# Kernel optimization log

Measured on AMD Instinct MI355X. Metric: run time of the kernel, lower is better.

## Reference

```python
import jax, jax.numpy as jnp
import numpy as np

B = 64           # number of graphs
MAXN = 128       # max nodes per graph (== to_dense_batch n)
D = 512          # hidden_dim
H = 16           # n_attn_heads
HS = D // H      # head_size
SCALE = HS ** -0.5
EPS = 1e-5

# deterministic ragged node counts in [64,128], max exactly 128
_COUNTS = 64 + (np.arange(B) * 37) % 65
NTOT = int(_COUNTS.sum())  # 6148


def setup_inputs() -> dict:
    key = jax.random.key(0)
    ks = jax.random.split(key, 10)
    r = D ** -0.5  # uniform init radius used by the module

    def lin(k):
        kw, kb = jax.random.split(k)
        W = jax.random.uniform(kw, (D, D), minval=-r, maxval=r, dtype=jnp.float32)
        b = jax.random.uniform(kb, (D,), minval=-r, maxval=r, dtype=jnp.float32)
        return W, b

    Wq, bq = lin(ks[0])
    Wk, bk = lin(ks[1])
    Wv, bv = lin(ks[2])
    Wp, bp = lin(ks[3])
    x = jax.random.normal(ks[4], (NTOT, D), dtype=jnp.float32)
    attn_bias = 0.1 * jax.random.normal(ks[5], (B, H, MAXN, MAXN), dtype=jnp.float32)
    batch = jnp.asarray(np.repeat(np.arange(B), _COUNTS), dtype=jnp.int32)
    return {
        "x": x, "attn_bias": attn_bias,
        "Wq": Wq, "bq": bq, "Wk": Wk, "bk": bk, "Wv": Wv, "bv": bv,
        "Wp": Wp, "bp": bp,
        "ln_w": jnp.ones((D,), jnp.float32), "ln_b": jnp.zeros((D,), jnp.float32),
        "batch": batch,
    }


def reference(x, attn_bias, Wq, bq, Wk, bk, Wv, bv, Wp, bp, ln_w, ln_b, batch):
    # eval-mode BiasedSelfAttentionLayer (all dropouts are identity)
    Bn, Hh, n, _ = attn_bias.shape
    N = x.shape[0]
    # to_dense_batch: per-node position inside its graph
    counts = jax.ops.segment_sum(jnp.ones(N, jnp.int32), batch, num_segments=Bn)
    starts = jnp.cumsum(counts) - counts
    pos = jnp.arange(N) - starts[batch]
    x_dense = jnp.zeros((Bn, n, D), x.dtype).at[batch, pos].set(x)  # [B,n,D]
    mask = jnp.zeros((Bn, n), bool).at[batch, pos].set(True)        # [B,n]

    def heads(W, b):
        return (x_dense @ W.T + b).reshape(Bn, n, Hh, HS).transpose(0, 2, 1, 3)

    q = heads(Wq, bq)  # [B,H,n,hs]
    k = heads(Wk, bk)
    v = heads(Wv, bv)

    attn = jnp.einsum("bhqd,bhkd->bhqk", q, k) * SCALE + attn_bias  # [B,H,n,n]
    mask2 = mask[:, None, :, None]  # valid queries
    mask3 = mask[:, None, None, :]  # valid keys
    attn = jnp.where(mask3, attn, -jnp.inf)   # masked_fill(~mask3, -inf)
    attn = jnp.where(mask2, attn, 0.0)        # masked_fill(~mask2, 0.0)
    attn = jax.nn.softmax(attn, axis=-1)
    attn = jnp.where(mask2, attn, 0.0)        # re-zero invalid query rows

    out = jnp.einsum("bhqk,bhkd->bhqd", attn, v)           # [B,H,n,hs]
    out = out.transpose(0, 2, 1, 3).reshape(Bn, n, D)      # [B,n,D]
    out = out @ Wp.T + bp
    out = out[batch, pos] + x                               # scatter back + residual
    # LayerNorm
    mu = out.mean(-1, keepdims=True)
    var = out.var(-1, keepdims=True)
    return (out - mu) / jnp.sqrt(var + EPS) * ln_w + ln_b
```

## Files before the change

kernel.cpp:

```cpp
#include <hip/hip_runtime.h>
#include <math.h>

#define NTOT 6148
#define NB 64
#define DM 512
#define SCALE_F 0.17677669529663687f

typedef __attribute__((ext_vector_type(8))) short bf16x8;
typedef __attribute__((ext_vector_type(4))) float f32x4;

__device__ __forceinline__ short f2bf(float f) {
  union { float f; unsigned u; } v; v.f = f;
  unsigned r = (v.u + 0x7fffu + ((v.u >> 16) & 1u)) >> 16;
  return (short)r;
}

__device__ __forceinline__ void gl_lds16(const void* g, void* l) {
  auto gp = (const __attribute__((address_space(1))) unsigned*)(unsigned long long)(uintptr_t)g;
  auto lp = (__attribute__((address_space(3))) unsigned*)(unsigned long long)(uintptr_t)l;
  __builtin_amdgcn_global_load_lds(gp, lp, 16, 0, 0);
}

__global__ __launch_bounds__(256) void k_starts(const int* __restrict__ batch,
                                                int* __restrict__ starts) {
  int i = blockIdx.x * 256 + threadIdx.x;
  if (i >= NTOT) return;
  int b = batch[i];
  if (i == 0) starts[b] = 0;
  else if (batch[i - 1] != b) starts[b] = i;
  if (i == NTOT - 1) starts[NB] = NTOT;
}

__global__ __launch_bounds__(256) void k_cvt(const float* __restrict__ x,
                                             const float* __restrict__ wq,
                                             const float* __restrict__ wk,
                                             const float* __restrict__ wv,
                                             const float* __restrict__ wp,
                                             short* __restrict__ xb,
                                             short* __restrict__ wqb,
                                             short* __restrict__ wkb,
                                             short* __restrict__ wvb,
                                             short* __restrict__ wpb) {
  const int bid = blockIdx.x;
  const float* s; short* d; long off;
  if (bid < 1537) {
    s = x; d = xb;
    off = ((long)bid * 256 + threadIdx.x) * 8;
  } else {
    int wi = (bid - 1537) >> 7;
    s = (wi == 0) ? wq : (wi == 1) ? wk : (wi == 2) ? wv : wp;
    d = (wi == 0) ? wqb : (wi == 1) ? wkb : (wi == 2) ? wvb : wpb;
    off = ((long)((bid - 1537) & 127) * 256 + threadIdx.x) * 8;
  }
  float4 v0 = *(const float4*)(s + off);
  float4 v1 = *(const float4*)(s + off + 4);
  bf16x8 o;
  o[0] = f2bf(v0.x); o[1] = f2bf(v0.y); o[2] = f2bf(v0.z); o[3] = f2bf(v0.w);
  o[4] = f2bf(v1.x); o[5] = f2bf(v1.y); o[6] = f2bf(v1.z); o[7] = f2bf(v1.w);
  *(bf16x8*)(d + off) = o;
}

template <int NT, bool BF16OUT>
__global__ __launch_bounds__(256) void k_gemm_mfma(
    const short* __restrict__ Abf,
    const short* __restrict__ W0, const short* __restrict__ W1, const short* __restrict__ W2,
    const float* __restrict__ b0, const float* __restrict__ b1, const float* __restrict__ b2,
    const float* __restrict__ resid, void* __restrict__ Cv, int ldc, int M) {
  constexpr int NF = NT / 32;
  __shared__ __align__(16) short As[2][64][32];
  __shared__ __align__(16) short Bs[2][NT][32];
  const int tid = threadIdx.x;
  const int w = tid >> 6, l = tid & 63;
  const int m0 = blockIdx.y * 64;
  const int n0 = blockIdx.x * NT;
  const int sel = n0 >> 9;
  const short* Wt = (sel == 0) ? W0 : (sel == 1) ? W1 : W2;
  const float* bt = (sel == 0) ? b0 : (sel == 1) ? b1 : b2;
  const int nl0 = n0 & 511;
  const int wr = w >> 1, wc = w & 1;
  const int lr = l >> 2;
  const int lc = (l & 3) * 8;
  const int fr = l & 15, fs = (l >> 4) * 8;

  const long gaA = (long)min(m0 + w * 16 + lr, M - 1) * 512 + lc;
  const long gaB0 = (long)(nl0 + ((NT == 128) ? w * 32 : w * 16) + lr) * 512 + lc;
  const long gaB1 = (long)(nl0 + w * 32 + 16 + lr) * 512 + lc;

  f32x4 acc[2][NF];
#pragma unroll
  for (int m = 0; m < 2; m++)
#pragma unroll
    for (int n = 0; n < NF; n++) acc[m][n] = (f32x4){0.f, 0.f, 0.f, 0.f};

  auto stage = [&](int kt, int buf) {
    const int k0 = kt * 32;
    gl_lds16(Abf + gaA + k0, &As[buf][w * 16][0]);
    if (NT == 128) {
      gl_lds16(Wt + gaB0 + k0, &Bs[buf][w * 32][0]);
      gl_lds16(Wt + gaB1 + k0, &Bs[buf][w * 32 + 16][0]);
    } else {
      gl_lds16(Wt + gaB0 + k0, &Bs[buf][w * 16][0]);
    }
  };
  auto compute = [&](int buf) {
    bf16x8 af[2], bfr[NF];
#pragma unroll
    for (int m = 0; m < 2; m++) af[m] = *(const bf16x8*)&As[buf][wr * 32 + m * 16 + fr][fs];
#pragma unroll
    for (int n = 0; n < NF; n++)
      bfr[n] = *(const bf16x8*)&Bs[buf][wc * (NT / 2) + n * 16 + fr][fs];
#pragma unroll
    for (int m = 0; m < 2; m++)
#pragma unroll
      for (int n = 0; n < NF; n++)
        acc[m][n] = __builtin_amdgcn_mfma_f32_16x16x32_bf16(af[m], bfr[n], acc[m][n], 0, 0, 0);
  };

  stage(0, 0);
  __syncthreads();
  for (int step = 0; step < 16; step++) {
    if (step < 15) stage(step + 1, (step + 1) & 1);
    compute(step & 1);
    __syncthreads();
  }

  const int er = (l >> 4) * 4, ec = l & 15;
#pragma unroll
  for (int n = 0; n < NF; n++) {
    const int col = n0 + wc * (NT / 2) + n * 16 + ec;
    const float bv = bt[col & 511];
#pragma unroll
    for (int m = 0; m < 2; m++) {
      const int rowb = m0 + wr * 32 + m * 16 + er;
#pragma unroll
      for (int j = 0; j < 4; j++) {
        const int row = rowb + j;
        if (row < M) {
          float v = acc[m][n][j] + bv;
          if (resid) v += resid[(long)row * 512 + col];
          if (BF16OUT) ((short*)Cv)[(long)row * ldc + col] = f2bf(v);
          else ((float*)Cv)[(long)row * ldc + col] = v;
        }
      }
    }
  }
}

__global__ __launch_bounds__(256, 2) void k_attn(const short* __restrict__ QKVbf,
                                                 const float* __restrict__ bias,
                                                 const int* __restrict__ starts,
                                                 short* __restrict__ Obf) {
  __shared__ __align__(16) float BiasP[4][16][264];
  __shared__ __align__(16) short Vtb[32][136];
  const int h = blockIdx.x, b = blockIdx.y;
  const int s0 = starts[b], cnt = starts[b + 1] - s0;
  const int tid = threadIdx.x, l = tid & 63, w = tid >> 6;
  const int wq0 = w * 32;
  const int lg = l >> 4, lk = l & 15, fs = lg * 8;
  const bool active = wq0 < cnt;
  short* Pw = (short*)&BiasP[w][0][0];

  const int u = l >> 2, c = (l & 3) * 8;
  const short* vbase = QKVbf + 1024 + h * 32 + c;
  const bf16x8 v0 = *(const bf16x8*)(vbase + (long)(s0 + min(wq0 + u, cnt - 1)) * 1536);
  const bf16x8 v1 = *(const bf16x8*)(vbase + (long)(s0 + min(wq0 + u + 16, cnt - 1)) * 1536);

  const float* bbase = bias + ((long)(b * 16 + h) << 14);
  if (active) {
    const float* bsrc = bbase + (long)wq0 * 128 + l * 4;
#pragma unroll
    for (int t = 0; t < 16; t++)
      gl_lds16(bsrc + t * 256, &BiasP[w][t][0]);
  }

  bf16x8 aq[2], bk[8];
  if (active) {
    const short* qbase = QKVbf + h * 32 + fs;
#pragma unroll
    for (int m = 0; m < 2; m++)
      aq[m] = *(const bf16x8*)(qbase + (long)(s0 + min(wq0 + m * 16 + lk, cnt - 1)) * 1536);
#pragma unroll
    for (int n = 0; n < 8; n++)
      bk[n] = *(const bf16x8*)(qbase + 512 + (long)(s0 + min(n * 16 + lk, cnt - 1)) * 1536);
  }

#pragma unroll
  for (int i = 0; i < 8; i++) Vtb[c + i][wq0 + u] = v0[i];
#pragma unroll
  for (int i = 0; i < 8; i++) Vtb[c + i][wq0 + u + 16] = v1[i];

  f32x4 S[2][8];
  float invs[2][4];
  if (active) {
#pragma unroll
    for (int n = 0; n < 8; n++)
#pragma unroll
      for (int m = 0; m < 2; m++)
        S[m][n] = __builtin_amdgcn_mfma_f32_16x16x32_bf16(aq[m], bk[n],
                                                          (f32x4){0.f, 0.f, 0.f, 0.f}, 0, 0, 0);
    asm volatile("s_waitcnt vmcnt(0)" ::: "memory");
    __builtin_amdgcn_sched_barrier(0);

#pragma unroll
    for (int m = 0; m < 2; m++) {
      const int rb = m * 16 + lg * 4;
#pragma unroll
      for (int n = 0; n < 8; n++) {
        const int k = n * 16 + lk;
        const bool kok = k < cnt;
#pragma unroll
        for (int j = 0; j < 4; j++) {
          const int r = rb + j;
          const float sv = S[m][n][j] * SCALE_F + BiasP[w][r >> 1][(r & 1) * 128 + k];
          S[m][n][j] = kok ? sv : -1e30f;
        }
      }
#pragma unroll
      for (int j = 0; j < 4; j++) {
        float mx = S[m][0][j];
#pragma unroll
        for (int n = 1; n < 8; n++) mx = fmaxf(mx, S[m][n][j]);
        mx = fmaxf(mx, __shfl_xor(mx, 1));
        mx = fmaxf(mx, __shfl_xor(mx, 2));
        mx = fmaxf(mx, __shfl_xor(mx, 4));
        mx = fmaxf(mx, __shfl_xor(mx, 8));
        float sum = 0.f;
#pragma unroll
        for (int n = 0; n < 8; n++) {
          const float p = __expf(S[m][n][j] - mx);
          S[m][n][j] = p;
          sum += p;
        }
        sum += __shfl_xor(sum, 1);
        sum += __shfl_xor(sum, 2);
        sum += __shfl_xor(sum, 4);
        sum += __shfl_xor(sum, 8);
        invs[m][j] = 1.f / sum;
        const int r = rb + j;
#pragma unroll
        for (int n = 0; n < 8; n++) Pw[r * 136 + n * 16 + lk] = f2bf(S[m][n][j]);
      }
    }
  }

  __syncthreads();
  if (!active) return;

  f32x4 O[2][2];
#pragma unroll
  for (int m = 0; m < 2; m++)
#pragma unroll
    for (int dt = 0; dt < 2; dt++) O[m][dt] = (f32x4){0.f, 0.f, 0.f, 0.f};
#pragma unroll
  for (int kc = 0; kc < 4; kc++) {
    bf16x8 pa[2], vb[2];
#pragma unroll
    for (int m = 0; m < 2; m++)
      pa[m] = *(const bf16x8*)&Pw[(m * 16 + lk) * 136 + kc * 32 + fs];
#pragma unroll
    for (int dt = 0; dt < 2; dt++) vb[dt] = *(const bf16x8*)&Vtb[dt * 16 + lk][kc * 32 + fs];
#pragma unroll
    for (int m = 0; m < 2; m++)
#pragma unroll
      for (int dt = 0; dt < 2; dt++)
        O[m][dt] = __builtin_amdgcn_mfma_f32_16x16x32_bf16(pa[m], vb[dt], O[m][dt], 0, 0, 0);
  }
#pragma unroll
  for (int m = 0; m < 2; m++) {
    const int qb0 = wq0 + m * 16 + lg * 4;
#pragma unroll
    for (int j = 0; j < 4; j++) {
      if (qb0 + j < cnt) {
        short* orow = Obf + (long)(s0 + qb0 + j) * 512 + h * 32;
#pragma unroll
        for (int dt = 0; dt < 2; dt++)
          orow[dt * 16 + lk] = f2bf(O[m][dt][j] * invs[m][j]);
      }
    }
  }
}

__global__ __launch_bounds__(256) void k_lnp(const float* __restrict__ pre,
                                             const float* __restrict__ lw,
                                             const float* __restrict__ lb,
                                             float* __restrict__ out) {
  const int row = blockIdx.x * 4 + (threadIdx.x >> 6);
  if (row >= NTOT) return;
  const int lane = threadIdx.x & 63;
  const float* pr = pre + (long)row * 512 + lane * 8;
  float4 p0 = *(const float4*)pr;
  float4 p1 = *(const float4*)(pr + 4);
  float v[8] = {p0.x, p0.y, p0.z, p0.w, p1.x, p1.y, p1.z, p1.w};
  float s = 0.f, s2 = 0.f;
#pragma unroll
  for (int j = 0; j < 8; j++) { s += v[j]; s2 += v[j] * v[j]; }
#pragma unroll
  for (int off = 32; off > 0; off >>= 1) {
    s += __shfl_xor(s, off);
    s2 += __shfl_xor(s2, off);
  }
  const float mu = s * (1.f / 512.f);
  const float var = s2 * (1.f / 512.f) - mu * mu;
  const float inv = rsqrtf(var + 1e-5f);
  float4 w0 = *(const float4*)&lw[lane * 8];
  float4 w1 = *(const float4*)&lw[lane * 8 + 4];
  float4 b0 = *(const float4*)&lb[lane * 8];
  float4 b1 = *(const float4*)&lb[lane * 8 + 4];
  float4 o0 = make_float4((v[0] - mu) * inv * w0.x + b0.x, (v[1] - mu) * inv * w0.y + b0.y,
                          (v[2] - mu) * inv * w0.z + b0.z, (v[3] - mu) * inv * w0.w + b0.w);
  float4 o1 = make_float4((v[4] - mu) * inv * w1.x + b1.x, (v[5] - mu) * inv * w1.y + b1.y,
                          (v[6] - mu) * inv * w1.z + b1.z, (v[7] - mu) * inv * w1.w + b1.w);
  float* dst = out + (long)row * 512 + lane * 8;
  *(float4*)dst = o0;
  *(float4*)(dst + 4) = o1;
}

extern "C" void kernel_launch(void* const* d_in, const int* in_sizes, int n_in,
                              void* d_out, int out_size, void* d_ws, size_t ws_size,
                              hipStream_t stream) {
  const float* x = (const float*)d_in[0];
  const float* attn_bias = (const float*)d_in[1];
  const float* Wq = (const float*)d_in[2];
  const float* bq = (const float*)d_in[3];
  const float* Wk = (const float*)d_in[4];
  const float* bk = (const float*)d_in[5];
  const float* Wv = (const float*)d_in[6];
  const float* bv = (const float*)d_in[7];
  const float* Wp = (const float*)d_in[8];
  const float* bp = (const float*)d_in[9];
  const float* ln_w = (const float*)d_in[10];
  const float* ln_b = (const float*)d_in[11];
  const int* batch = (const int*)d_in[12];
  float* out = (float*)d_out;

  char* ws = (char*)d_ws;
  int* starts = (int*)ws;
  short* Xbf = (short*)(ws + 512);
  short* Wqb = Xbf + (long)NTOT * 512;
  short* Wkb = Wqb + 512 * 512;
  short* Wvb = Wkb + 512 * 512;
  short* Wpb = Wvb + 512 * 512;
  short* QKVbf = Wpb + 512 * 512;
  short* Obf = Xbf;
  float* proj = (float*)QKVbf;

  k_starts<<<(NTOT + 255) / 256, 256, 0, stream>>>(batch, starts);
  k_cvt<<<1537 + 4 * 128, 256, 0, stream>>>(x, Wq, Wk, Wv, Wp, Xbf, Wqb, Wkb, Wvb, Wpb);

  dim3 gq(12, (NTOT + 63) / 64);
  k_gemm_mfma<128, true><<<gq, 256, 0, stream>>>(Xbf, Wqb, Wkb, Wvb, bq, bk, bv,
                                                 nullptr, QKVbf, 1536, NTOT);

  dim3 ga(16, NB);
  k_attn<<<ga, 256, 0, stream>>>(QKVbf, attn_bias, starts, Obf);

  dim3 gp(8, (NTOT + 63) / 64);
  k_gemm_mfma<64, false><<<gp, 256, 0, stream>>>(Obf, Wpb, Wpb, Wpb, bp, bp, bp,
                                                 x, proj, 512, NTOT);

  k_lnp<<<(NTOT + 3) / 4, 256, 0, stream>>>(proj, ln_w, ln_b, out);
}
```

Before: 85.40 us.

## Split attention block into 8 waves of 16 query rows each

The attention kernel now launches 512 threads per (head, graph) block, with each of eight waves handling 16 query rows instead of four waves handling 32. Per-wave register use (S, O, aq) is halved, and the bias prefetch into LDS is issued unconditionally at kernel start, before the starts lookup. The aim is more wave-level parallelism and latency hiding for the bias loads and softmax. In exchange, the K fragments are loaded redundantly by twice as many waves, and inactive waves still prefetch bias.

Measured after the change: 83.47 us. 2.3% less time.

```diff
diff --git a/kernel.cpp b/kernel.cpp
--- a/kernel.cpp
+++ b/kernel.cpp
@@ -146,39 +146,36 @@
   }
 }
 
-__global__ __launch_bounds__(256, 2) void k_attn(const short* __restrict__ QKVbf,
+__global__ __launch_bounds__(512, 4) void k_attn(const short* __restrict__ QKVbf,
                                                  const float* __restrict__ bias,
                                                  const int* __restrict__ starts,
                                                  short* __restrict__ Obf) {
-  __shared__ __align__(16) float BiasP[4][16][264];
+  __shared__ __align__(16) float BiasP[8][8][264];
   __shared__ __align__(16) short Vtb[32][136];
   const int h = blockIdx.x, b = blockIdx.y;
+  const int tid = threadIdx.x, l = tid & 63, w = tid >> 6;
+  const int wq0 = w * 16;
+  const int lg = l >> 4, lk = l & 15, fs = lg * 8;
+  short* Pw = (short*)&BiasP[w][0][0];
+
+  {
+    const float* bsrc = bias + ((long)(b * 16 + h) << 14) + (long)wq0 * 128 + l * 4;
+#pragma unroll
+    for (int t = 0; t < 8; t++)
+      gl_lds16(bsrc + t * 256, &BiasP[w][t][0]);
+  }
+
   const int s0 = starts[b], cnt = starts[b + 1] - s0;
-  const int tid = threadIdx.x, l = tid & 63, w = tid >> 6;
-  const int wq0 = w * 32;
-  const int lg = l >> 4, lk = l & 15, fs = lg * 8;
   const bool active = wq0 < cnt;
-  short* Pw = (short*)&BiasP[w][0][0];
 
   const int u = l >> 2, c = (l & 3) * 8;
   const short* vbase = QKVbf + 1024 + h * 32 + c;
   const bf16x8 v0 = *(const bf16x8*)(vbase + (long)(s0 + min(wq0 + u, cnt - 1)) * 1536);
-  const bf16x8 v1 = *(const bf16x8*)(vbase + (long)(s0 + min(wq0 + u + 16, cnt - 1)) * 1536);
-
-  const float* bbase = bias + ((long)(b * 16 + h) << 14);
-  if (active) {
-    const float* bsrc = bbase + (long)wq0 * 128 + l * 4;
-#pragma unroll
-    for (int t = 0; t < 16; t++)
-      gl_lds16(bsrc + t * 256, &BiasP[w][t][0]);
-  }
-
-  bf16x8 aq[2], bk[8];
+
+  bf16x8 aq, bk[8];
   if (active) {
     const short* qbase = QKVbf + h * 32 + fs;
-#pragma unroll
-    for (int m = 0; m < 2; m++)
-      aq[m] = *(const bf16x8*)(qbase + (long)(s0 + min(wq0 + m * 16 + lk, cnt - 1)) * 1536);
+    aq = *(const bf16x8*)(qbase + (long)(s0 + min(wq0 + lk, cnt - 1)) * 1536);
 #pragma unroll
     for (int n = 0; n < 8; n++)
       bk[n] = *(const bf16x8*)(qbase + 512 + (long)(s0 + min(n * 16 + lk, cnt - 1)) * 1536);
@@ -186,96 +183,78 @@
 
 #pragma unroll
   for (int i = 0; i < 8; i++) Vtb[c + i][wq0 + u] = v0[i];
-#pragma unroll
-  for (int i = 0; i < 8; i++) Vtb[c + i][wq0 + u + 16] = v1[i];
-
-  f32x4 S[2][8];
-  float invs[2][4];
+
+  asm volatile("s_waitcnt vmcnt(0)" ::: "memory");
+  __builtin_amdgcn_sched_barrier(0);
+
+  f32x4 S[8];
+  float invs[4];
   if (active) {
 #pragma unroll
     for (int n = 0; n < 8; n++)
-#pragma unroll
-      for (int m = 0; m < 2; m++)
-        S[m][n] = __builtin_amdgcn_mfma_f32_16x16x32_bf16(aq[m], bk[n],
-                                                          (f32x4){0.f, 0.f, 0.f, 0.f}, 0, 0, 0);
-    asm volatile("s_waitcnt vmcnt(0)" ::: "memory");
-    __builtin_amdgcn_sched_barrier(0);
-
-#pragma unroll
-    for (int m = 0; m < 2; m++) {
-      const int rb = m * 16 + lg * 4;
+      S[n] = __builtin_amdgcn_mfma_f32_16x16x32_bf16(aq, bk[n],
+                                                     (f32x4){0.f, 0.f, 0.f, 0.f}, 0, 0, 0);
+#pragma unroll
+    for (int n = 0; n < 8; n++) {
+      const int k = n * 16 + lk;
+      const bool kok = k < cnt;
+#pragma unroll
+      for (int j = 0; j < 4; j++) {
+        const int r = lg * 4 + j;
+        const float sv = S[n][j] * SCALE_F + BiasP[w][r >> 1][(r & 1) * 128 + k];
+        S[n][j] = kok ? sv : -1e30f;
+      }
+    }
+#pragma unroll
+    for (int j = 0; j < 4; j++) {
+      float mx = S[0][j];
+#pragma unroll
+      for (int n = 1; n < 8; n++) mx = fmaxf(mx, S[n][j]);
+      mx = fmaxf(mx, __shfl_xor(mx, 1));
+      mx = fmaxf(mx, __shfl_xor(mx, 2));
+      mx = fmaxf(mx, __shfl_xor(mx, 4));
+      mx = fmaxf(mx, __shfl_xor(mx, 8));
+      float sum = 0.f;
 #pragma unroll
       for (int n = 0; n < 8; n++) {
-        const int k = n * 16 + lk;
-        const bool kok = k < cnt;
-#pragma unroll
-        for (int j = 0; j < 4; j++) {
-          const int r = rb + j;
-          const float sv = S[m][n][j] * SCALE_F + BiasP[w][r >> 1][(r & 1) * 128 + k];
-          S[m][n][j] = kok ? sv : -1e30f;
-        }
+        const float p = __expf(S[n][j] - mx);
+        S[n][j] = p;
+        sum += p;
       }
-#pragma unroll
-      for (int j = 0; j < 4; j++) {
-        float mx = S[m][0][j];
-#pragma unroll
-        for (int n = 1; n < 8; n++) mx = fmaxf(mx, S[m][n][j]);
-        mx = fmaxf(mx, __shfl_xor(mx, 1));
-        mx = fmaxf(mx, __shfl_xor(mx, 2));
-        mx = fmaxf(mx, __shfl_xor(mx, 4));
-        mx = fmaxf(mx, __shfl_xor(mx, 8));
-        float sum = 0.f;
-#pragma unroll
-        for (int n = 0; n < 8; n++) {
-          const float p = __expf(S[m][n][j] - mx);
-          S[m][n][j] = p;
-          sum += p;
-        }
-        sum += __shfl_xor(sum, 1);
-        sum += __shfl_xor(sum, 2);
-        sum += __shfl_xor(sum, 4);
-        sum += __shfl_xor(sum, 8);
-        invs[m][j] = 1.f / sum;
-        const int r = rb + j;
-#pragma unroll
-        for (int n = 0; n < 8; n++) Pw[r * 136 + n * 16 + lk] = f2bf(S[m][n][j]);
-      }
+      sum += __shfl_xor(sum, 1);
+      sum += __shfl_xor(sum, 2);
+      sum += __shfl_xor(sum, 4);
+      sum += __shfl_xor(sum, 8);
+      invs[j] = 1.f / sum;
+      const int r = lg * 4 + j;
+#pragma unroll
+      for (int n = 0; n < 8; n++) Pw[r * 136 + n * 16 + lk] = f2bf(S[n][j]);
     }
   }
 
   __syncthreads();
   if (!active) return;
 
-  f32x4 O[2][2];
-#pragma unroll
-  for (int m = 0; m < 2; m++)
-#pragma unroll
-    for (int dt = 0; dt < 2; dt++) O[m][dt] = (f32x4){0.f, 0.f, 0.f, 0.f};
+  f32x4 O[2];
+#pragma unroll
+  for (int dt = 0; dt < 2; dt++) O[dt] = (f32x4){0.f, 0.f, 0.f, 0.f};
 #pragma unroll
   for (int kc = 0; kc < 4; kc++) {
-    bf16x8 pa[2], vb[2];
-#pragma unroll
-    for (int m = 0; m < 2; m++)
-      pa[m] = *(const bf16x8*)&Pw[(m * 16 + lk) * 136 + kc * 32 + fs];
-#pragma unroll
-    for (int dt = 0; dt < 2; dt++) vb[dt] = *(const bf16x8*)&Vtb[dt * 16 + lk][kc * 32 + fs];
-#pragma unroll
-    for (int m = 0; m < 2; m++)
+    const bf16x8 pa = *(const bf16x8*)&Pw[lk * 136 + kc * 32 + fs];
+#pragma unroll
+    for (int dt = 0; dt < 2; dt++) {
+      const bf16x8 vb = *(const bf16x8*)&Vtb[dt * 16 + lk][kc * 32 + fs];
+      O[dt] = __builtin_amdgcn_mfma_f32_16x16x32_bf16(pa, vb, O[dt], 0, 0, 0);
+    }
+  }
+#pragma unroll
+  for (int j = 0; j < 4; j++) {
+    const int q = wq0 + lg * 4 + j;
+    if (q < cnt) {
+      short* orow = Obf + (long)(s0 + q) * 512 + h * 32;
 #pragma unroll
       for (int dt = 0; dt < 2; dt++)
-        O[m][dt] = __builtin_amdgcn_mfma_f32_16x16x32_bf16(pa[m], vb[dt], O[m][dt], 0, 0, 0);
-  }
-#pragma unroll
-  for (int m = 0; m < 2; m++) {
-    const int qb0 = wq0 + m * 16 + lg * 4;
-#pragma unroll
-    for (int j = 0; j < 4; j++) {
-      if (qb0 + j < cnt) {
-        short* orow = Obf + (long)(s0 + qb0 + j) * 512 + h * 32;
-#pragma unroll
-        for (int dt = 0; dt < 2; dt++)
-          orow[dt * 16 + lk] = f2bf(O[m][dt][j] * invs[m][j]);
-      }
+        orow[dt * 16 + lk] = f2bf(O[dt][j] * invs[j]);
     }
   }
 }
@@ -352,7 +331,7 @@
                                                  nullptr, QKVbf, 1536, NTOT);
 
   dim3 ga(16, NB);
-  k_attn<<<ga, 256, 0, stream>>>(QKVbf, attn_bias, starts, Obf);
+  k_attn<<<ga, 512, 0, stream>>>(QKVbf, attn_bias, starts, Obf);
 
   dim3 gp(8, (NTOT + 63) / 64);
   k_gemm_mfma<64, false><<<gp, 256, 0, stream>>>(Obf, Wpb, Wpb, Wpb, bp, bp, bp,
```
